# Optimization experiments

Measured on AMD Instinct MI355X. Metric: run time of the kernel, lower is better.

## Reference

```python
import jax, jax.numpy as jnp
import numpy as np
from jax import lax

T = 262144
H = 64
OUT = 16  # 2**MEMORY_LENGTH with MEMORY_LENGTH=4


def setup_inputs() -> dict:
    key = jax.random.key(0)
    ks = jax.random.split(key, 11)
    s = 0.1  # keep gates out of saturation
    return {
        "y": jax.random.normal(ks[0], (T, 1), jnp.float32),
        "W_ih0": s * jax.random.normal(ks[1], (4 * H, 1), jnp.float32),
        "W_hh0": s * jax.random.normal(ks[2], (4 * H, H), jnp.float32),
        "b_ih0": s * jax.random.normal(ks[3], (4 * H,), jnp.float32),
        "b_hh0": s * jax.random.normal(ks[4], (4 * H,), jnp.float32),
        "W_ih1": s * jax.random.normal(ks[5], (4 * H, H), jnp.float32),
        "W_hh1": s * jax.random.normal(ks[6], (4 * H, H), jnp.float32),
        "b_ih1": s * jax.random.normal(ks[7], (4 * H,), jnp.float32),
        "b_hh1": s * jax.random.normal(ks[8], (4 * H,), jnp.float32),
        "W_lin": s * jax.random.normal(ks[9], (OUT, H), jnp.float32),
        "b_lin": s * jax.random.normal(ks[10], (OUT,), jnp.float32),
    }


def _lstm_layer(x, W_ih, W_hh, b_ih, b_hh):
    # x: [T, in]. PyTorch gate order: i, f, g, o. Zero initial state.
    h = W_hh.shape[1]
    xp = x @ W_ih.T + (b_ih + b_hh)  # precompute input contribution: [T, 4H]

    def step(carry, xt):
        h_t, c_t = carry
        gates = xt + h_t @ W_hh.T
        i, f, g, o = jnp.split(gates, 4)
        i = jax.nn.sigmoid(i)
        f = jax.nn.sigmoid(f)
        g = jnp.tanh(g)
        o = jax.nn.sigmoid(o)
        c_new = f * c_t + i * g
        h_new = o * jnp.tanh(c_new)
        return (h_new, c_new), h_new

    init = (jnp.zeros((h,), x.dtype), jnp.zeros((h,), x.dtype))
    _, hs = lax.scan(step, init, xp)
    return hs  # [T, H]


def reference(y, W_ih0, W_hh0, b_ih0, b_hh0, W_ih1, W_hh1, b_ih1, b_hh1, W_lin, b_lin):
    # phase == 'train' branch of RNNDetector.forward
    h1 = _lstm_layer(y, W_ih0, W_hh0, b_ih0, b_hh0)   # [T, 64]
    h2 = _lstm_layer(h1, W_ih1, W_hh1, b_ih1, b_hh1)  # [T, 64]
    return h2 @ W_lin.T + b_lin                        # [T, 16]
```

## Files before the change

kernel.cpp:

```cpp
#include <hip/hip_runtime.h>


constexpr int T  = 262144;
constexpr int B  = 32;
constexpr int NB = T / B;
constexpr int RS = 2 * B;
constexpr int K_SS = NB + 3;

typedef _Float16 h2v __attribute__((ext_vector_type(2)));
typedef unsigned u4 __attribute__((ext_vector_type(4)));

__device__ __forceinline__ float rcp_f(float x) { return __builtin_amdgcn_rcpf(x); }

#define BARRIER() asm volatile("s_waitcnt lgkmcnt(0)\n\ts_barrier" ::: "memory")

static __device__ __forceinline__ float fd(unsigned w, unsigned h, float acc) {
#if __has_builtin(__builtin_amdgcn_fdot2)
  return __builtin_amdgcn_fdot2(__builtin_bit_cast(h2v, w),
                                __builtin_bit_cast(h2v, h), acc, false);
#else
  h2v a = __builtin_bit_cast(h2v, w), b = __builtin_bit_cast(h2v, h);
  acc = fmaf((float)a.x, (float)b.x, acc);
  acc = fmaf((float)a.y, (float)b.y, acc);
  return acc;
#endif
}

#define DP4(acc, W, H) { acc = fd((W).x, (H).x, acc); acc = fd((W).y, (H).y, acc); \
                         acc = fd((W).z, (H).z, acc); acc = fd((W).w, (H).w, acc); }

#define DPPX1(x) __builtin_bit_cast(float, __builtin_amdgcn_mov_dpp(            \
                    __builtin_bit_cast(int, (x)), 0xB1, 0xF, 0xF, true))
#define DPPX2(x) __builtin_bit_cast(float, __builtin_amdgcn_mov_dpp(            \
                    __builtin_bit_cast(int, (x)), 0x4E, 0xF, 0xF, true))

__device__ __forceinline__ float sigf(float x) {
  float z = fminf(fmaxf(x, -30.f), 30.f);
  return rcp_f(1.f + __expf(-z));
}
__device__ __forceinline__ float tanhf_(float x) {
  float z = fminf(fmaxf(x, -15.f), 15.f);
  float e2 = __expf(-2.f * z);
  return (1.f - e2) * rcp_f(1.f + e2);
}

__device__ unsigned f16rne(float f) {
  unsigned u = __float_as_uint(f);
  unsigned s = (u >> 16) & 0x8000u;
  int e = (int)((u >> 23) & 0xff) - 127;
  unsigned m = u & 0x7fffffu;
  if (e < -14) return s;
  unsigned h = s | (unsigned)((e + 15) << 10) | (m >> 13);
  unsigned rem = m & 0x1fffu;
  h += (rem > 0x1000u) || (rem == 0x1000u && (h & 1u));
  return h;
}

__global__ void pack_w(const float* __restrict__ Whh0,
                       const float* __restrict__ Whh1,
                       const float* __restrict__ Wih1,
                       const float* __restrict__ Wlin,
                       unsigned* __restrict__ ws) {
  int i = blockIdx.x * 256 + threadIdx.x;
  if (i >= 25088) return;
  float v0, v1;
  if (i < 24576) {
    int w = i >> 13, rem = i & 8191, l = rem >> 7, d = rem & 127;
    int r = d >> 5, kp = d & 31, row = r * 64 + l;
    const float* src = (w == 0) ? Whh0 : (w == 1) ? Whh1 : Wih1;
    v0 = src[row * 64 + 2 * kp]; v1 = src[row * 64 + 2 * kp + 1];
  } else {
    int j = i - 24576, l = j >> 3, d = j & 7;
    int m = l >> 2, kq = l & 3, k = kq * 16 + 2 * d;
    v0 = Wlin[m * 64 + k]; v1 = Wlin[m * 64 + k + 1];
  }
  ws[i] = f16rne(v0) | (f16rne(v1) << 16);
}

#define DECLW32(wp)                                                            \
  u4 W0=(wp)[0],  W1=(wp)[1],  W2=(wp)[2],  W3=(wp)[3],                        \
     W4=(wp)[4],  W5=(wp)[5],  W6=(wp)[6],  W7=(wp)[7],                        \
     W8=(wp)[8],  W9=(wp)[9],  W10=(wp)[10],W11=(wp)[11],                      \
     W12=(wp)[12],W13=(wp)[13],W14=(wp)[14],W15=(wp)[15],                      \
     W16=(wp)[16],W17=(wp)[17],W18=(wp)[18],W19=(wp)[19],                      \
     W20=(wp)[20],W21=(wp)[21],W22=(wp)[22],W23=(wp)[23],                      \
     W24=(wp)[24],W25=(wp)[25],W26=(wp)[26],W27=(wp)[27],                      \
     W28=(wp)[28],W29=(wp)[29],W30=(wp)[30],W31=(wp)[31]

#define PINW8(a,b,c,d,e,f,g,h)                                                 \
  asm volatile("" : "+v"(a), "+v"(b), "+v"(c), "+v"(d),                        \
                    "+v"(e), "+v"(f), "+v"(g), "+v"(h))
#define PINALL() { PINW8(W0,W1,W2,W3,W4,W5,W6,W7);                             \
                   PINW8(W8,W9,W10,W11,W12,W13,W14,W15);                       \
                   PINW8(W16,W17,W18,W19,W20,W21,W22,W23);                     \
                   PINW8(W24,W25,W26,W27,W28,W29,W30,W31); }

__global__ __launch_bounds__(192)
__attribute__((amdgpu_waves_per_eu(1, 1)))
void rnn_fused(
    const float* __restrict__ y,
    const float* __restrict__ Wih0, const float* __restrict__ bih0,
    const float* __restrict__ bhh0,
    const float* __restrict__ bih1, const float* __restrict__ bhh1,
    const float* __restrict__ blin,
    const unsigned* __restrict__ ws,
    float* __restrict__ out)
{
  const int tid = threadIdx.x;
  __shared__ __align__(16) unsigned h0r[RS * 32];
  __shared__ __align__(16) unsigned h1r[RS * 32];
  __shared__ __align__(16) float    xp[RS * 256];

  for (int j = tid; j < RS * 32; j += 192) { h0r[j] = 0u; h1r[j] = 0u; }
  __syncthreads();

  if (tid < 64) {
    const int e = tid;
    const u4* wp = (const u4*)(ws + e * 128);
    DECLW32(wp);
    float bbi = bih0[e] + bhh0[e];
    float bbf = bih0[64 + e] + bhh0[64 + e];
    float bbg = bih0[128 + e] + bhh0[128 + e];
    float bbo = bih0[192 + e] + bhh0[192 + e];
    float wii = Wih0[e], wif = Wih0[64 + e], wig = Wih0[128 + e], wio = Wih0[192 + e];
    float c0 = 0.f;
    float ylv = y[e & (B - 1)];

    for (int k = 0; k < K_SS; ++k) {
      if (k < NB) {
        float yln = (k + 1 < NB) ? y[(k + 1) * B + (e & (B - 1))] : 0.f;
        const int base = k * B;
        #pragma unroll 1
        for (int i = 0; i < B; ++i) {
          const int s = base + i;
          PINALL();
          const u4* hp = (const u4*)(h0r + ((s - 1) & (RS - 1)) * 32);
          u4 H0=hp[0],H1=hp[1],H2=hp[2],H3=hp[3],H4=hp[4],H5=hp[5],H6=hp[6],H7=hp[7];
          float ys = __builtin_bit_cast(float,
              __builtin_amdgcn_readlane(__builtin_bit_cast(int, ylv), i));
          float ai0=0,ai1=0, af0=0,af1=0, ag0=0,ag1=0, ao0=0,ao1=0;
          DP4(ai0,W0,H0)  DP4(af0,W8,H0)  DP4(ag0,W16,H0) DP4(ao0,W24,H0)
          DP4(ai1,W1,H1)  DP4(af1,W9,H1)  DP4(ag1,W17,H1) DP4(ao1,W25,H1)
          DP4(ai0,W2,H2)  DP4(af0,W10,H2) DP4(ag0,W18,H2) DP4(ao0,W26,H2)
          DP4(ai1,W3,H3)  DP4(af1,W11,H3) DP4(ag1,W19,H3) DP4(ao1,W27,H3)
          DP4(ai0,W4,H4)  DP4(af0,W12,H4) DP4(ag0,W20,H4) DP4(ao0,W28,H4)
          DP4(ai1,W5,H5)  DP4(af1,W13,H5) DP4(ag1,W21,H5) DP4(ao1,W29,H5)
          DP4(ai0,W6,H6)  DP4(af0,W14,H6) DP4(ag0,W22,H6) DP4(ao0,W30,H6)
          DP4(ai1,W7,H7)  DP4(af1,W15,H7) DP4(ag1,W23,H7) DP4(ao1,W31,H7)
          float I = sigf((ai0 + ai1) + fmaf(ys, wii, bbi));
          float F = sigf((af0 + af1) + fmaf(ys, wif, bbf));
          float G = tanhf_((ag0 + ag1) + fmaf(ys, wig, bbg));
          float O = sigf((ao0 + ao1) + fmaf(ys, wio, bbo));
          c0 = fmaf(F, c0, I * G);
          float h = O * tanhf_(c0);
          float hp1 = DPPX1(h);
          unsigned pk = __builtin_bit_cast(unsigned, __builtin_amdgcn_cvt_pkrtz(h, hp1));
          if (!(e & 1)) h0r[(s & (RS - 1)) * 32 + (e >> 1)] = pk;
        }
        ylv = yln;
      }
      BARRIER();
    }
  } else if (tid < 128) {
    const int e = tid - 64;
    const u4* wp = (const u4*)(ws + 16384 + e * 128);
    DECLW32(wp);
    const u4* hwp = (const u4*)(ws + 24576 + e * 8);
    u4 HW0 = hwp[0], HW1 = hwp[1];
    float bb0 = bih1[e] + bhh1[e];
    float bb1 = bih1[64 + e] + bhh1[64 + e];
    float bb2 = bih1[128 + e] + bhh1[128 + e];
    float bb3 = bih1[192 + e] + bhh1[192 + e];
    const int m = e >> 2, kq = e & 3;
    float bl = (kq == 0) ? blin[m] : 0.f;

    for (int k = 0; k < K_SS; ++k) {
      if (k >= 1 && k <= NB) {
        const int base = (k - 1) * B;
        #pragma unroll 1
        for (int i = 0; i < B; ++i) {
          const int t = base + i;
          const int slot = t & (RS - 1);
          PINALL();
          const u4* hp = (const u4*)(h0r + slot * 32);
          u4 H0=hp[0],H1=hp[1],H2=hp[2],H3=hp[3],H4=hp[4],H5=hp[5],H6=hp[6],H7=hp[7];
          float p0a=0,p0b=0, p1a=0,p1b=0, p2a=0,p2b=0, p3a=0,p3b=0;
          DP4(p0a,W0,H0) DP4(p1a,W8,H0)  DP4(p2a,W16,H0) DP4(p3a,W24,H0)
          DP4(p0b,W1,H1) DP4(p1b,W9,H1)  DP4(p2b,W17,H1) DP4(p3b,W25,H1)
          DP4(p0a,W2,H2) DP4(p1a,W10,H2) DP4(p2a,W18,H2) DP4(p3a,W26,H2)
          DP4(p0b,W3,H3) DP4(p1b,W11,H3) DP4(p2b,W19,H3) DP4(p3b,W27,H3)
          DP4(p0a,W4,H4) DP4(p1a,W12,H4) DP4(p2a,W20,H4) DP4(p3a,W28,H4)
          DP4(p0b,W5,H5) DP4(p1b,W13,H5) DP4(p2b,W21,H5) DP4(p3b,W29,H5)
          DP4(p0a,W6,H6) DP4(p1a,W14,H6) DP4(p2a,W22,H6) DP4(p3a,W30,H6)
          DP4(p0b,W7,H7) DP4(p1b,W15,H7) DP4(p2b,W23,H7) DP4(p3b,W31,H7)
          float* xq = xp + slot * 256;
          xq[e]       = (p0a + p0b) + bb0;
          xq[64 + e]  = (p1a + p1b) + bb1;
          xq[128 + e] = (p2a + p2b) + bb2;
          xq[192 + e] = (p3a + p3b) + bb3;
        }
      }
      if (k >= 3) {
        const int base = (k - 3) * B;
        #pragma unroll 1
        for (int i = 0; i < B; ++i) {
          const int t = base + i;
          const int slot = t & (RS - 1);
          const u4* h1p = (const u4*)(h1r + slot * 32 + kq * 8);
          u4 X0 = h1p[0], X1 = h1p[1];
          float r2 = 0.f;
          DP4(r2, HW0, X0) DP4(r2, HW1, X1)
          r2 += DPPX1(r2);
          r2 += DPPX2(r2);
          if (kq == 0) out[t * 16 + m] = r2 + bl;
        }
      }
      BARRIER();
    }
  } else {
    const int e = tid - 128;
    const u4* wp = (const u4*)(ws + 8192 + e * 128);
    DECLW32(wp);
    float c1 = 0.f;

    for (int k = 0; k < K_SS; ++k) {
      if (k >= 2 && k <= NB + 1) {
        const int base = (k - 2) * B;
        #pragma unroll 1
        for (int i = 0; i < B; ++i) {
          const int t = base + i;
          const int slot = t & (RS - 1);
          PINALL();
          const u4* hp = (const u4*)(h1r + ((t - 1) & (RS - 1)) * 32);
          u4 H0=hp[0],H1=hp[1],H2=hp[2],H3=hp[3],H4=hp[4],H5=hp[5],H6=hp[6],H7=hp[7];
          float ai0=0,ai1=0, af0=0,af1=0, ag0=0,ag1=0, ao0=0,ao1=0;
          DP4(ai0,W0,H0)  DP4(af0,W8,H0)  DP4(ag0,W16,H0) DP4(ao0,W24,H0)
          DP4(ai1,W1,H1)  DP4(af1,W9,H1)  DP4(ag1,W17,H1) DP4(ao1,W25,H1)
          DP4(ai0,W2,H2)  DP4(af0,W10,H2) DP4(ag0,W18,H2) DP4(ao0,W26,H2)
          DP4(ai1,W3,H3)  DP4(af1,W11,H3) DP4(ag1,W19,H3) DP4(ao1,W27,H3)
          DP4(ai0,W4,H4)  DP4(af0,W12,H4) DP4(ag0,W20,H4) DP4(ao0,W28,H4)
          DP4(ai1,W5,H5)  DP4(af1,W13,H5) DP4(ag1,W21,H5) DP4(ao1,W29,H5)
          DP4(ai0,W6,H6)  DP4(af0,W14,H6) DP4(ag0,W22,H6) DP4(ao0,W30,H6)
          DP4(ai1,W7,H7)  DP4(af1,W15,H7) DP4(ag1,W23,H7) DP4(ao1,W31,H7)
          const float* xq = xp + slot * 256;
          float xi = xq[e], xf = xq[64 + e], xg = xq[128 + e], xo = xq[192 + e];
          float I = sigf(xi + (ai0 + ai1));
          float F = sigf(xf + (af0 + af1));
          float G = tanhf_(xg + (ag0 + ag1));
          float O = sigf(xo + (ao0 + ao1));
          c1 = fmaf(F, c1, I * G);
          float h = O * tanhf_(c1);
          float hp1 = DPPX1(h);
          unsigned pk = __builtin_bit_cast(unsigned, __builtin_amdgcn_cvt_pkrtz(h, hp1));
          if (!(e & 1)) h1r[slot * 32 + (e >> 1)] = pk;
        }
      }
      BARRIER();
    }
  }
}

extern "C" void kernel_launch(void* const* d_in, const int* in_sizes, int n_in,
                              void* d_out, int out_size, void* d_ws, size_t ws_size,
                              hipStream_t stream) {
  const float* y    = (const float*)d_in[0];
  const float* Wih0 = (const float*)d_in[1];
  const float* Whh0 = (const float*)d_in[2];
  const float* bih0 = (const float*)d_in[3];
  const float* bhh0 = (const float*)d_in[4];
  const float* Wih1 = (const float*)d_in[5];
  const float* Whh1 = (const float*)d_in[6];
  const float* bih1 = (const float*)d_in[7];
  const float* bhh1 = (const float*)d_in[8];
  const float* Wlin = (const float*)d_in[9];
  const float* blin = (const float*)d_in[10];
  unsigned* ws = (unsigned*)d_ws;

  pack_w<<<dim3(98), dim3(256), 0, stream>>>(Whh0, Whh1, Wih1, Wlin, ws);
  rnn_fused<<<dim3(1), dim3(192), 0, stream>>>(
      y, Wih0, bih0, bhh0, bih1, bhh1, blin, ws, (float*)d_out);
}
```

Before: 117.5 ms.

## Split fused LSTM pipeline across three cooperative workgroups with global-memory flag handoff

Replaces the single 192-thread workgroup with three cooperatively launched workgroups: one runs the layer-0 recurrence, one computes layer-1 input projections and the output linear, and one runs the layer-1 recurrence. Hidden states and projected inputs pass between workgroups through ring buffers in global memory, synchronized with release/acquire counters and spin-waits. Each recurrence workgroup has a second wave that moves data between LDS and global memory. The aim is to stop the two recurrences and the projection work from sharing one CU and its barriers. The cost is cross-CU latency, more global traffic and spin-wait overhead.

```diff
diff --git a/kernel.cpp b/kernel.cpp
--- a/kernel.cpp
+++ b/kernel.cpp
@@ -4,8 +4,11 @@
 constexpr int T  = 262144;
 constexpr int B  = 32;
 constexpr int NB = T / B;
-constexpr int RS = 2 * B;
-constexpr int K_SS = NB + 3;
+
+constexpr int H0G = 25600;  constexpr int H0_RING = 8;
+constexpr int H1G = 33792;  constexpr int H1_RING = 8;
+constexpr int XPG = 41984;  constexpr int XP_RING = 4;
+constexpr int CNT = 74752;
 
 typedef _Float16 h2v __attribute__((ext_vector_type(2)));
 typedef unsigned u4 __attribute__((ext_vector_type(4)));
@@ -44,6 +47,20 @@
   return (1.f - e2) * rcp_f(1.f + e2);
 }
 
+__device__ __forceinline__ void ag_store(unsigned* p, unsigned v) {
+  __hip_atomic_store(p, v, __ATOMIC_RELAXED, __HIP_MEMORY_SCOPE_AGENT);
+}
+__device__ __forceinline__ unsigned ag_load(const unsigned* p) {
+  return __hip_atomic_load(p, __ATOMIC_RELAXED, __HIP_MEMORY_SCOPE_AGENT);
+}
+__device__ __forceinline__ void flag_set(int* p, int v) {
+  __hip_atomic_store(p, v, __ATOMIC_RELEASE, __HIP_MEMORY_SCOPE_AGENT);
+}
+__device__ __forceinline__ void waitge(int* p, int tgt) {
+  while (__hip_atomic_load(p, __ATOMIC_ACQUIRE, __HIP_MEMORY_SCOPE_AGENT) < tgt)
+    __builtin_amdgcn_s_sleep(8);
+}
+
 __device__ unsigned f16rne(float f) {
   unsigned u = __float_as_uint(f);
   unsigned s = (u >> 16) & 0x8000u;
@@ -61,6 +78,7 @@
                        const float* __restrict__ Wih1,
                        const float* __restrict__ Wlin,
                        unsigned* __restrict__ ws) {
+  if (blockIdx.x == 0 && threadIdx.x < 4) ws[CNT + threadIdx.x] = 0u;
   int i = blockIdx.x * 256 + threadIdx.x;
   if (i >= 25088) return;
   float v0, v1;
@@ -95,7 +113,7 @@
                    PINW8(W16,W17,W18,W19,W20,W21,W22,W23);                     \
                    PINW8(W24,W25,W26,W27,W28,W29,W30,W31); }
 
-__global__ __launch_bounds__(192)
+__global__ __launch_bounds__(128)
 __attribute__((amdgpu_waves_per_eu(1, 1)))
 void rnn_fused(
     const float* __restrict__ y,
@@ -103,38 +121,36 @@
     const float* __restrict__ bhh0,
     const float* __restrict__ bih1, const float* __restrict__ bhh1,
     const float* __restrict__ blin,
-    const unsigned* __restrict__ ws,
+    unsigned* __restrict__ wsu,
     float* __restrict__ out)
 {
-  const int tid = threadIdx.x;
-  __shared__ __align__(16) unsigned h0r[RS * 32];
-  __shared__ __align__(16) unsigned h1r[RS * 32];
-  __shared__ __align__(16) float    xp[RS * 256];
-
-  for (int j = tid; j < RS * 32; j += 192) { h0r[j] = 0u; h1r[j] = 0u; }
+  const int tid  = threadIdx.x;
+  const int role = blockIdx.x;
+  int* cnt = (int*)(wsu + CNT);
+
+  __shared__ __align__(16) unsigned smem[18432];
+  for (int j = tid; j < 2048; j += 128) smem[j] = 0u;
   __syncthreads();
 
-  if (tid < 64) {
-    const int e = tid;
-    const u4* wp = (const u4*)(ws + e * 128);
-    DECLW32(wp);
-    float bbi = bih0[e] + bhh0[e];
-    float bbf = bih0[64 + e] + bhh0[64 + e];
-    float bbg = bih0[128 + e] + bhh0[128 + e];
-    float bbo = bih0[192 + e] + bhh0[192 + e];
-    float wii = Wih0[e], wif = Wih0[64 + e], wig = Wih0[128 + e], wio = Wih0[192 + e];
-    float c0 = 0.f;
-    float ylv = y[e & (B - 1)];
-
-    for (int k = 0; k < K_SS; ++k) {
-      if (k < NB) {
+  if (role == 0) {
+    if (tid < 64) {
+      const int e = tid;
+      const u4* wp = (const u4*)(wsu + e * 128);
+      DECLW32(wp);
+      float bbi = bih0[e] + bhh0[e];
+      float bbf = bih0[64 + e] + bhh0[64 + e];
+      float bbg = bih0[128 + e] + bhh0[128 + e];
+      float bbo = bih0[192 + e] + bhh0[192 + e];
+      float wii = Wih0[e], wif = Wih0[64 + e], wig = Wih0[128 + e], wio = Wih0[192 + e];
+      float c0 = 0.f;
+      float ylv = y[e & (B - 1)];
+      for (int k = 0; k < NB; ++k) {
         float yln = (k + 1 < NB) ? y[(k + 1) * B + (e & (B - 1))] : 0.f;
-        const int base = k * B;
         #pragma unroll 1
         for (int i = 0; i < B; ++i) {
-          const int s = base + i;
+          const int s = k * B + i;
           PINALL();
-          const u4* hp = (const u4*)(h0r + ((s - 1) & (RS - 1)) * 32);
+          const u4* hp = (const u4*)(smem + ((s - 1) & 63) * 32);
           u4 H0=hp[0],H1=hp[1],H2=hp[2],H3=hp[3],H4=hp[4],H5=hp[5],H6=hp[6],H7=hp[7];
           float ys = __builtin_bit_cast(float,
               __builtin_amdgcn_readlane(__builtin_bit_cast(int, ylv), i));
@@ -155,17 +171,42 @@
           float h = O * tanhf_(c0);
           float hp1 = DPPX1(h);
           unsigned pk = __builtin_bit_cast(unsigned, __builtin_amdgcn_cvt_pkrtz(h, hp1));
-          if (!(e & 1)) h0r[(s & (RS - 1)) * 32 + (e >> 1)] = pk;
+          if (!(e & 1)) smem[(s & 63) * 32 + (e >> 1)] = pk;
         }
         ylv = yln;
-      }
+        BARRIER();
+      }
+      BARRIER();
+    } else {
+      const int l = tid - 64;
+      auto export_h0 = [&](int kb) {
+        if (kb >= H0_RING) waitge(cnt + 1, kb - H0_RING + 1);
+        const u4* src = (const u4*)(smem + (kb & 1) * 1024 + l * 16);
+        u4 A0 = src[0], A1 = src[1], A2 = src[2], A3 = src[3];
+        unsigned* dst = wsu + H0G + (kb & (H0_RING - 1)) * 1024 + l * 16;
+        ag_store(dst + 0,  A0.x); ag_store(dst + 1,  A0.y);
+        ag_store(dst + 2,  A0.z); ag_store(dst + 3,  A0.w);
+        ag_store(dst + 4,  A1.x); ag_store(dst + 5,  A1.y);
+        ag_store(dst + 6,  A1.z); ag_store(dst + 7,  A1.w);
+        ag_store(dst + 8,  A2.x); ag_store(dst + 9,  A2.y);
+        ag_store(dst + 10, A2.z); ag_store(dst + 11, A2.w);
+        ag_store(dst + 12, A3.x); ag_store(dst + 13, A3.y);
+        ag_store(dst + 14, A3.z); ag_store(dst + 15, A3.w);
+        __threadfence();
+        if (l == 0) flag_set(cnt + 0, kb + 1);
+      };
+      for (int k = 0; k < NB; ++k) {
+        if (k >= 1) export_h0(k - 1);
+        BARRIER();
+      }
+      export_h0(NB - 1);
       BARRIER();
     }
-  } else if (tid < 128) {
-    const int e = tid - 64;
-    const u4* wp = (const u4*)(ws + 16384 + e * 128);
+  } else if (role == 1) {
+    const int w = tid >> 6, e = tid & 63;
+    const u4* wp = (const u4*)(wsu + 16384 + e * 128);
     DECLW32(wp);
-    const u4* hwp = (const u4*)(ws + 24576 + e * 8);
+    const u4* hwp = (const u4*)(wsu + 24576 + e * 8);
     u4 HW0 = hwp[0], HW1 = hwp[1];
     float bb0 = bih1[e] + bhh1[e];
     float bb1 = bih1[64 + e] + bhh1[64 + e];
@@ -174,15 +215,32 @@
     const int m = e >> 2, kq = e & 3;
     float bl = (kq == 0) ? blin[m] : 0.f;
 
-    for (int k = 0; k < K_SS; ++k) {
-      if (k >= 1 && k <= NB) {
-        const int base = (k - 1) * B;
-        #pragma unroll 1
-        for (int i = 0; i < B; ++i) {
-          const int t = base + i;
-          const int slot = t & (RS - 1);
+    for (int j = 0; j < NB + 2; ++j) {
+      if (j < NB) {
+        waitge(cnt + 0, j + 1);
+        const unsigned* g = wsu + H0G + (j & (H0_RING - 1)) * 1024 + tid * 8;
+        unsigned d0 = ag_load(g + 0), d1 = ag_load(g + 1), d2 = ag_load(g + 2), d3 = ag_load(g + 3);
+        unsigned d4 = ag_load(g + 4), d5 = ag_load(g + 5), d6 = ag_load(g + 6), d7 = ag_load(g + 7);
+        u4 P0 = {d0, d1, d2, d3}, P1 = {d4, d5, d6, d7};
+        *(u4*)(smem + tid * 8) = P0;
+        *(u4*)(smem + tid * 8 + 4) = P1;
+      }
+      if (j >= 2) {
+        waitge(cnt + 2, j - 1);
+        const unsigned* g = wsu + H1G + ((j - 2) & (H1_RING - 1)) * 1024 + tid * 8;
+        unsigned d0 = ag_load(g + 0), d1 = ag_load(g + 1), d2 = ag_load(g + 2), d3 = ag_load(g + 3);
+        unsigned d4 = ag_load(g + 4), d5 = ag_load(g + 5), d6 = ag_load(g + 6), d7 = ag_load(g + 7);
+        u4 P0 = {d0, d1, d2, d3}, P1 = {d4, d5, d6, d7};
+        *(u4*)(smem + 1024 + tid * 8) = P0;
+        *(u4*)(smem + 1024 + tid * 8 + 4) = P1;
+      }
+      __syncthreads();
+      if (j < NB) {
+        unsigned* xq0 = wsu + XPG + (j & (XP_RING - 1)) * 8192;
+        #pragma unroll 1
+        for (int i = w * 16; i < w * 16 + 16; ++i) {
           PINALL();
-          const u4* hp = (const u4*)(h0r + slot * 32);
+          const u4* hp = (const u4*)(smem + i * 32);
           u4 H0=hp[0],H1=hp[1],H2=hp[2],H3=hp[3],H4=hp[4],H5=hp[5],H6=hp[6],H7=hp[7];
           float p0a=0,p0b=0, p1a=0,p1b=0, p2a=0,p2b=0, p3a=0,p3b=0;
           DP4(p0a,W0,H0) DP4(p1a,W8,H0)  DP4(p2a,W16,H0) DP4(p3a,W24,H0)
@@ -193,45 +251,45 @@
           DP4(p0b,W5,H5) DP4(p1b,W13,H5) DP4(p2b,W21,H5) DP4(p3b,W29,H5)
           DP4(p0a,W6,H6) DP4(p1a,W14,H6) DP4(p2a,W22,H6) DP4(p3a,W30,H6)
           DP4(p0b,W7,H7) DP4(p1b,W15,H7) DP4(p2b,W23,H7) DP4(p3b,W31,H7)
-          float* xq = xp + slot * 256;
-          xq[e]       = (p0a + p0b) + bb0;
-          xq[64 + e]  = (p1a + p1b) + bb1;
-          xq[128 + e] = (p2a + p2b) + bb2;
-          xq[192 + e] = (p3a + p3b) + bb3;
-        }
-      }
-      if (k >= 3) {
-        const int base = (k - 3) * B;
-        #pragma unroll 1
-        for (int i = 0; i < B; ++i) {
-          const int t = base + i;
-          const int slot = t & (RS - 1);
-          const u4* h1p = (const u4*)(h1r + slot * 32 + kq * 8);
+          unsigned* xq = xq0 + i * 256;
+          ag_store(xq + e,       __float_as_uint((p0a + p0b) + bb0));
+          ag_store(xq + 64 + e,  __float_as_uint((p1a + p1b) + bb1));
+          ag_store(xq + 128 + e, __float_as_uint((p2a + p2b) + bb2));
+          ag_store(xq + 192 + e, __float_as_uint((p3a + p3b) + bb3));
+        }
+      }
+      if (j >= 2) {
+        const int tb = (j - 2) * B;
+        #pragma unroll 1
+        for (int i = w * 16; i < w * 16 + 16; ++i) {
+          const u4* h1p = (const u4*)(smem + 1024 + i * 32 + kq * 8);
           u4 X0 = h1p[0], X1 = h1p[1];
           float r2 = 0.f;
           DP4(r2, HW0, X0) DP4(r2, HW1, X1)
           r2 += DPPX1(r2);
           r2 += DPPX2(r2);
-          if (kq == 0) out[t * 16 + m] = r2 + bl;
-        }
-      }
-      BARRIER();
+          if (kq == 0) out[(tb + i) * 16 + m] = r2 + bl;
+        }
+      }
+      __threadfence();
+      __syncthreads();
+      if (tid == 0 && j < NB) flag_set(cnt + 1, j + 1);
+      if (tid == 64 && j >= 2) flag_set(cnt + 3, j - 1);
     }
   } else {
-    const int e = tid - 128;
-    const u4* wp = (const u4*)(ws + 8192 + e * 128);
-    DECLW32(wp);
-    float c1 = 0.f;
-
-    for (int k = 0; k < K_SS; ++k) {
-      if (k >= 2 && k <= NB + 1) {
-        const int base = (k - 2) * B;
+    if (tid < 64) {
+      const int e = tid;
+      const u4* wp = (const u4*)(wsu + 8192 + e * 128);
+      DECLW32(wp);
+      float c1 = 0.f;
+      BARRIER();
+      for (int k = 0; k < NB; ++k) {
+        const float* xqb = (const float*)(smem + 2048 + (k & 1) * 8192);
         #pragma unroll 1
         for (int i = 0; i < B; ++i) {
-          const int t = base + i;
-          const int slot = t & (RS - 1);
+          const int t = k * B + i;
           PINALL();
-          const u4* hp = (const u4*)(h1r + ((t - 1) & (RS - 1)) * 32);
+          const u4* hp = (const u4*)(smem + ((t - 1) & 63) * 32);
           u4 H0=hp[0],H1=hp[1],H2=hp[2],H3=hp[3],H4=hp[4],H5=hp[5],H6=hp[6],H7=hp[7];
           float ai0=0,ai1=0, af0=0,af1=0, ag0=0,ag1=0, ao0=0,ao1=0;
           DP4(ai0,W0,H0)  DP4(af0,W8,H0)  DP4(ag0,W16,H0) DP4(ao0,W24,H0)
@@ -242,7 +300,7 @@
           DP4(ai1,W5,H5)  DP4(af1,W13,H5) DP4(ag1,W21,H5) DP4(ao1,W29,H5)
           DP4(ai0,W6,H6)  DP4(af0,W14,H6) DP4(ag0,W22,H6) DP4(ao0,W30,H6)
           DP4(ai1,W7,H7)  DP4(af1,W15,H7) DP4(ag1,W23,H7) DP4(ao1,W31,H7)
-          const float* xq = xp + slot * 256;
+          const float* xq = xqb + i * 256;
           float xi = xq[e], xf = xq[64 + e], xg = xq[128 + e], xo = xq[192 + e];
           float I = sigf(xi + (ai0 + ai1));
           float F = sigf(xf + (af0 + af1));
@@ -252,9 +310,58 @@
           float h = O * tanhf_(c1);
           float hp1 = DPPX1(h);
           unsigned pk = __builtin_bit_cast(unsigned, __builtin_amdgcn_cvt_pkrtz(h, hp1));
-          if (!(e & 1)) h1r[slot * 32 + (e >> 1)] = pk;
-        }
-      }
+          if (!(e & 1)) smem[(t & 63) * 32 + (e >> 1)] = pk;
+        }
+        BARRIER();
+      }
+      BARRIER();
+    } else {
+      const int l = tid - 64;
+      auto stage_xp = [&](int blk) {
+        const unsigned* g = wsu + XPG + (blk & (XP_RING - 1)) * 8192 + l * 128;
+        unsigned* d = smem + 2048 + (blk & 1) * 8192 + l * 128;
+        #pragma unroll 1
+        for (int c0 = 0; c0 < 32; c0 += 8) {
+          u4 P[8];
+          #pragma unroll
+          for (int q = 0; q < 8; ++q) {
+            P[q].x = ag_load(g + (c0 + q) * 4 + 0);
+            P[q].y = ag_load(g + (c0 + q) * 4 + 1);
+            P[q].z = ag_load(g + (c0 + q) * 4 + 2);
+            P[q].w = ag_load(g + (c0 + q) * 4 + 3);
+          }
+          #pragma unroll
+          for (int q = 0; q < 8; ++q) *(u4*)(d + (c0 + q) * 4) = P[q];
+        }
+      };
+      auto export_h1 = [&](int kb, int cval) {
+        if (kb >= H1_RING) waitge(cnt + 3, kb - H1_RING + 1);
+        const u4* src = (const u4*)(smem + (kb & 1) * 1024 + l * 16);
+        u4 A0 = src[0], A1 = src[1], A2 = src[2], A3 = src[3];
+        unsigned* dst = wsu + H1G + (kb & (H1_RING - 1)) * 1024 + l * 16;
+        ag_store(dst + 0,  A0.x); ag_store(dst + 1,  A0.y);
+        ag_store(dst + 2,  A0.z); ag_store(dst + 3,  A0.w);
+        ag_store(dst + 4,  A1.x); ag_store(dst + 5,  A1.y);
+        ag_store(dst + 6,  A1.z); ag_store(dst + 7,  A1.w);
+        ag_store(dst + 8,  A2.x); ag_store(dst + 9,  A2.y);
+        ag_store(dst + 10, A2.z); ag_store(dst + 11, A2.w);
+        ag_store(dst + 12, A3.x); ag_store(dst + 13, A3.y);
+        ag_store(dst + 14, A3.z); ag_store(dst + 15, A3.w);
+        __threadfence();
+        if (l == 0) flag_set(cnt + 2, cval);
+      };
+      waitge(cnt + 1, 1);
+      stage_xp(0);
+      BARRIER();
+      for (int k = 0; k < NB; ++k) {
+        if (k >= 1) export_h1(k - 1, k);
+        if (k + 1 < NB) {
+          waitge(cnt + 1, k + 2);
+          stage_xp(k + 1);
+        }
+        BARRIER();
+      }
+      export_h1(NB - 1, NB);
       BARRIER();
     }
   }
@@ -275,8 +382,12 @@
   const float* Wlin = (const float*)d_in[9];
   const float* blin = (const float*)d_in[10];
   unsigned* ws = (unsigned*)d_ws;
+  float* outp = (float*)d_out;
 
   pack_w<<<dim3(98), dim3(256), 0, stream>>>(Whh0, Whh1, Wih1, Wlin, ws);
-  rnn_fused<<<dim3(1), dim3(192), 0, stream>>>(
-      y, Wih0, bih0, bhh0, bih1, bhh1, blin, ws, (float*)d_out);
-}
+
+  void* args[] = {(void*)&y, (void*)&Wih0, (void*)&bih0, (void*)&bhh0,
+                  (void*)&bih1, (void*)&bhh1, (void*)&blin, (void*)&ws,
+                  (void*)&outp};
+  hipLaunchCooperativeKernel((void*)rnn_fused, dim3(3), dim3(128), args, 0, stream);
+}
```

Measured after the change: 126.8 ms. +7.9%, slower.

## Fold log2(e) into weights and use raw v_exp, b16 stores, vector xp loads

Applied to the files above, without the earlier changes.

Pre-scales the recurrent and input weights and biases by log2(e), or 2*log2(e) for the g gate, so the gate activations can call v_exp_f32 directly. This removes the clamps and the multiply inside each sigmoid and tanh on the serial recurrence path. The h outputs are now written as single f16 stores per lane instead of a DPP exchange plus a packed store. The xp buffer is re-laid out so each lane moves its four gate pre-activations with one 16-byte access, and the two recurrent waves get raised scheduling priority. The risk is small numeric drift from rounding the scaled weights to f16 and from the altered clamping of large arguments.

```diff
diff --git a/kernel.cpp b/kernel.cpp
--- a/kernel.cpp
+++ b/kernel.cpp
@@ -9,6 +9,7 @@
 
 typedef _Float16 h2v __attribute__((ext_vector_type(2)));
 typedef unsigned u4 __attribute__((ext_vector_type(4)));
+typedef float    f4 __attribute__((ext_vector_type(4)));
 
 __device__ __forceinline__ float rcp_f(float x) { return __builtin_amdgcn_rcpf(x); }
 
@@ -34,15 +35,25 @@
 #define DPPX2(x) __builtin_bit_cast(float, __builtin_amdgcn_mov_dpp(            \
                     __builtin_bit_cast(int, (x)), 0x4E, 0xF, 0xF, true))
 
-__device__ __forceinline__ float sigf(float x) {
-  float z = fminf(fmaxf(x, -30.f), 30.f);
-  return rcp_f(1.f + __expf(-z));
-}
-__device__ __forceinline__ float tanhf_(float x) {
-  float z = fminf(fmaxf(x, -15.f), 15.f);
-  float e2 = __expf(-2.f * z);
+__device__ __forceinline__ float exp2_f(float x) {
+  float r; asm("v_exp_f32 %0, %1" : "=v"(r) : "v"(x)); return r;
+}
+__device__ __forceinline__ float exp2n_g(float u) {
+  return exp2_f(fminf(-u, 126.f));
+}
+__device__ __forceinline__ float sig_u(float u) {
+  return rcp_f(1.f + exp2n_g(u));
+}
+__device__ __forceinline__ float tanh_u(float u) {
+  float e2 = exp2n_g(u);
   return (1.f - e2) * rcp_f(1.f + e2);
 }
+__device__ __forceinline__ float tanh_c(float c) {
+  return tanh_u(c * 2.8853900817779268f);
+}
+
+constexpr float L2E  = 1.4426950408889634f;
+constexpr float L2E2 = 2.8853900817779268f;
 
 __device__ unsigned f16rne(float f) {
   unsigned u = __float_as_uint(f);
@@ -63,18 +74,19 @@
                        unsigned* __restrict__ ws) {
   int i = blockIdx.x * 256 + threadIdx.x;
   if (i >= 25088) return;
-  float v0, v1;
+  float v0, v1, sc = 1.f;
   if (i < 24576) {
     int w = i >> 13, rem = i & 8191, l = rem >> 7, d = rem & 127;
     int r = d >> 5, kp = d & 31, row = r * 64 + l;
     const float* src = (w == 0) ? Whh0 : (w == 1) ? Whh1 : Wih1;
     v0 = src[row * 64 + 2 * kp]; v1 = src[row * 64 + 2 * kp + 1];
+    sc = (r == 2) ? L2E2 : L2E;
   } else {
     int j = i - 24576, l = j >> 3, d = j & 7;
     int m = l >> 2, kq = l & 3, k = kq * 16 + 2 * d;
     v0 = Wlin[m * 64 + k]; v1 = Wlin[m * 64 + k + 1];
   }
-  ws[i] = f16rne(v0) | (f16rne(v1) << 16);
+  ws[i] = f16rne(v0 * sc) | (f16rne(v1 * sc) << 16);
 }
 
 #define DECLW32(wp)                                                            \
@@ -109,22 +121,25 @@
   const int tid = threadIdx.x;
   __shared__ __align__(16) unsigned h0r[RS * 32];
   __shared__ __align__(16) unsigned h1r[RS * 32];
-  __shared__ __align__(16) float    xp[RS * 256];
+  __shared__ __align__(16) float    xpf[RS * 256];
 
   for (int j = tid; j < RS * 32; j += 192) { h0r[j] = 0u; h1r[j] = 0u; }
   __syncthreads();
 
   if (tid < 64) {
+    __builtin_amdgcn_s_setprio(1);
     const int e = tid;
     const u4* wp = (const u4*)(ws + e * 128);
     DECLW32(wp);
-    float bbi = bih0[e] + bhh0[e];
-    float bbf = bih0[64 + e] + bhh0[64 + e];
-    float bbg = bih0[128 + e] + bhh0[128 + e];
-    float bbo = bih0[192 + e] + bhh0[192 + e];
-    float wii = Wih0[e], wif = Wih0[64 + e], wig = Wih0[128 + e], wio = Wih0[192 + e];
+    float bbi = (bih0[e] + bhh0[e]) * L2E;
+    float bbf = (bih0[64 + e] + bhh0[64 + e]) * L2E;
+    float bbg = (bih0[128 + e] + bhh0[128 + e]) * L2E2;
+    float bbo = (bih0[192 + e] + bhh0[192 + e]) * L2E;
+    float wii = Wih0[e] * L2E, wif = Wih0[64 + e] * L2E;
+    float wig = Wih0[128 + e] * L2E2, wio = Wih0[192 + e] * L2E;
     float c0 = 0.f;
     float ylv = y[e & (B - 1)];
+    _Float16* h0h = (_Float16*)h0r;
 
     for (int k = 0; k < K_SS; ++k) {
       if (k < NB) {
@@ -134,10 +149,10 @@
         for (int i = 0; i < B; ++i) {
           const int s = base + i;
           PINALL();
+          float ys = __builtin_bit_cast(float,
+              __builtin_amdgcn_readlane(__builtin_bit_cast(int, ylv), i));
           const u4* hp = (const u4*)(h0r + ((s - 1) & (RS - 1)) * 32);
           u4 H0=hp[0],H1=hp[1],H2=hp[2],H3=hp[3],H4=hp[4],H5=hp[5],H6=hp[6],H7=hp[7];
-          float ys = __builtin_bit_cast(float,
-              __builtin_amdgcn_readlane(__builtin_bit_cast(int, ylv), i));
           float ai0=0,ai1=0, af0=0,af1=0, ag0=0,ag1=0, ao0=0,ao1=0;
           DP4(ai0,W0,H0)  DP4(af0,W8,H0)  DP4(ag0,W16,H0) DP4(ao0,W24,H0)
           DP4(ai1,W1,H1)  DP4(af1,W9,H1)  DP4(ag1,W17,H1) DP4(ao1,W25,H1)
@@ -147,15 +162,13 @@
           DP4(ai1,W5,H5)  DP4(af1,W13,H5) DP4(ag1,W21,H5) DP4(ao1,W29,H5)
           DP4(ai0,W6,H6)  DP4(af0,W14,H6) DP4(ag0,W22,H6) DP4(ao0,W30,H6)
           DP4(ai1,W7,H7)  DP4(af1,W15,H7) DP4(ag1,W23,H7) DP4(ao1,W31,H7)
-          float I = sigf((ai0 + ai1) + fmaf(ys, wii, bbi));
-          float F = sigf((af0 + af1) + fmaf(ys, wif, bbf));
-          float G = tanhf_((ag0 + ag1) + fmaf(ys, wig, bbg));
-          float O = sigf((ao0 + ao1) + fmaf(ys, wio, bbo));
+          float I = sig_u((ai0 + ai1) + fmaf(ys, wii, bbi));
+          float F = sig_u((af0 + af1) + fmaf(ys, wif, bbf));
+          float G = tanh_u((ag0 + ag1) + fmaf(ys, wig, bbg));
+          float O = sig_u((ao0 + ao1) + fmaf(ys, wio, bbo));
           c0 = fmaf(F, c0, I * G);
-          float h = O * tanhf_(c0);
-          float hp1 = DPPX1(h);
-          unsigned pk = __builtin_bit_cast(unsigned, __builtin_amdgcn_cvt_pkrtz(h, hp1));
-          if (!(e & 1)) h0r[(s & (RS - 1)) * 32 + (e >> 1)] = pk;
+          float h = O * tanh_c(c0);
+          h0h[(s & (RS - 1)) * 64 + e] = (_Float16)h;
         }
         ylv = yln;
       }
@@ -167,10 +180,10 @@
     DECLW32(wp);
     const u4* hwp = (const u4*)(ws + 24576 + e * 8);
     u4 HW0 = hwp[0], HW1 = hwp[1];
-    float bb0 = bih1[e] + bhh1[e];
-    float bb1 = bih1[64 + e] + bhh1[64 + e];
-    float bb2 = bih1[128 + e] + bhh1[128 + e];
-    float bb3 = bih1[192 + e] + bhh1[192 + e];
+    float bb0 = (bih1[e] + bhh1[e]) * L2E;
+    float bb1 = (bih1[64 + e] + bhh1[64 + e]) * L2E;
+    float bb2 = (bih1[128 + e] + bhh1[128 + e]) * L2E2;
+    float bb3 = (bih1[192 + e] + bhh1[192 + e]) * L2E;
     const int m = e >> 2, kq = e & 3;
     float bl = (kq == 0) ? blin[m] : 0.f;
 
@@ -193,11 +206,12 @@
           DP4(p0b,W5,H5) DP4(p1b,W13,H5) DP4(p2b,W21,H5) DP4(p3b,W29,H5)
           DP4(p0a,W6,H6) DP4(p1a,W14,H6) DP4(p2a,W22,H6) DP4(p3a,W30,H6)
           DP4(p0b,W7,H7) DP4(p1b,W15,H7) DP4(p2b,W23,H7) DP4(p3b,W31,H7)
-          float* xq = xp + slot * 256;
-          xq[e]       = (p0a + p0b) + bb0;
-          xq[64 + e]  = (p1a + p1b) + bb1;
-          xq[128 + e] = (p2a + p2b) + bb2;
-          xq[192 + e] = (p3a + p3b) + bb3;
+          f4 v;
+          v.x = (p0a + p0b) + bb0;
+          v.y = (p1a + p1b) + bb1;
+          v.z = (p2a + p2b) + bb2;
+          v.w = (p3a + p3b) + bb3;
+          *(f4*)(xpf + slot * 256 + e * 4) = v;
         }
       }
       if (k >= 3) {
@@ -218,10 +232,12 @@
       BARRIER();
     }
   } else {
+    __builtin_amdgcn_s_setprio(1);
     const int e = tid - 128;
     const u4* wp = (const u4*)(ws + 8192 + e * 128);
     DECLW32(wp);
     float c1 = 0.f;
+    _Float16* h1h = (_Float16*)h1r;
 
     for (int k = 0; k < K_SS; ++k) {
       if (k >= 2 && k <= NB + 1) {
@@ -231,6 +247,7 @@
           const int t = base + i;
           const int slot = t & (RS - 1);
           PINALL();
+          const f4 xq = *(const f4*)(xpf + slot * 256 + e * 4);
           const u4* hp = (const u4*)(h1r + ((t - 1) & (RS - 1)) * 32);
           u4 H0=hp[0],H1=hp[1],H2=hp[2],H3=hp[3],H4=hp[4],H5=hp[5],H6=hp[6],H7=hp[7];
           float ai0=0,ai1=0, af0=0,af1=0, ag0=0,ag1=0, ao0=0,ao1=0;
@@ -242,17 +259,13 @@
           DP4(ai1,W5,H5)  DP4(af1,W13,H5) DP4(ag1,W21,H5) DP4(ao1,W29,H5)
           DP4(ai0,W6,H6)  DP4(af0,W14,H6) DP4(ag0,W22,H6) DP4(ao0,W30,H6)
           DP4(ai1,W7,H7)  DP4(af1,W15,H7) DP4(ag1,W23,H7) DP4(ao1,W31,H7)
-          const float* xq = xp + slot * 256;
-          float xi = xq[e], xf = xq[64 + e], xg = xq[128 + e], xo = xq[192 + e];
-          float I = sigf(xi + (ai0 + ai1));
-          float F = sigf(xf + (af0 + af1));
-          float G = tanhf_(xg + (ag0 + ag1));
-          float O = sigf(xo + (ao0 + ao1));
+          float I = sig_u(xq.x + (ai0 + ai1));
+          float F = sig_u(xq.y + (af0 + af1));
+          float G = tanh_u(xq.z + (ag0 + ag1));
+          float O = sig_u(xq.w + (ao0 + ao1));
           c1 = fmaf(F, c1, I * G);
-          float h = O * tanhf_(c1);
-          float hp1 = DPPX1(h);
-          unsigned pk = __builtin_bit_cast(unsigned, __builtin_amdgcn_cvt_pkrtz(h, hp1));
-          if (!(e & 1)) h1r[slot * 32 + (e >> 1)] = pk;
+          float h = O * tanh_c(c1);
+          h1h[slot * 64 + e] = (_Float16)h;
         }
       }
       BARRIER();
```

New measurement: 114.8 ms. -2.3%, faster.
